# Kernel optimization log

Measured on AMD Instinct MI355X. Metric: run time of the kernel, lower is better.

The kernel has to match this reference:

```python
import jax, jax.numpy as jnp
import numpy as np

N0, N1, N2 = 262144, 65536, 16384   # sampled src nodes, layer-1 targets, layer-2 targets
E1, E2 = 1048576, 262144            # fanout 16 edges per layer
IN_C, HID_C, OUT_C = 128, 256, 64


def sage_conv(x_src, x_dst, src, dst, num_dst, W_l, W_r, b):
    # PyG SAGEConv (mean aggr): out = mean_{j in N(i)} x_src[j] @ W_l^T + b + x_dst @ W_r^T
    msgs = x_src[src]                                   # [E, C] gather
    s = jax.ops.segment_sum(msgs, dst, num_segments=num_dst)
    cnt = jax.ops.segment_sum(jnp.ones((src.shape[0],), x_src.dtype), dst,
                              num_segments=num_dst)
    aggr = s / jnp.maximum(cnt, 1.0)[:, None]           # mean; isolated nodes -> 0
    return aggr @ W_l.T + b + x_dst @ W_r.T


def setup_inputs() -> dict:
    key = jax.random.key(0)
    ks = jax.random.split(key, 9)
    inp = {
        "x": jax.random.normal(ks[0], (N0, IN_C), dtype=jnp.float32),
        "src1": jax.random.randint(ks[1], (E1,), 0, N0, dtype=jnp.int32),
        "dst1": jax.random.randint(ks[2], (E1,), 0, N1, dtype=jnp.int32),
        "src2": jax.random.randint(ks[3], (E2,), 0, N1, dtype=jnp.int32),
        "dst2": jax.random.randint(ks[4], (E2,), 0, N2, dtype=jnp.int32),
        "W1_l": jax.random.normal(ks[5], (HID_C, IN_C), dtype=jnp.float32) * 0.05,
        "W1_r": jax.random.normal(ks[6], (HID_C, IN_C), dtype=jnp.float32) * 0.05,
        "b1": jnp.zeros((HID_C,), dtype=jnp.float32),
        "W2_l": jax.random.normal(ks[7], (OUT_C, HID_C), dtype=jnp.float32) * 0.05,
        "W2_r": jax.random.normal(ks[8], (OUT_C, HID_C), dtype=jnp.float32) * 0.05,
        "b2": jnp.zeros((OUT_C,), dtype=jnp.float32),
    }
    return inp


def reference(x, src1, dst1, src2, dst2, W1_l, W1_r, b1, W2_l, W2_r, b2):
    # layer 1: sources = all N0 nodes, targets = first N1 nodes (x_target = x[:size[1]])
    h = sage_conv(x, x[:N1], src1, dst1, N1, W1_l, W1_r, b1)   # [N1, HID_C]
    h = jax.nn.relu(h)   # dropout is identity in eval mode
    # layer 2: sources = N1 layer-1 outputs, targets = first N2
    h = sage_conv(h, h[:N2], src2, dst2, N2, W2_l, W2_r, b2)   # [N2, OUT_C]
    return jax.nn.log_softmax(h, axis=-1)
```

## Files before the change

### kernel.cpp

```cpp
#include <hip/hip_runtime.h>
#include <cstdint>
#include <cstddef>

#define N0C 262144
#define N1C 65536
#define N2C 16384
#define E1C 1048576
#define E2C 262144

typedef __attribute__((ext_vector_type(8))) short bf16x8;
typedef __attribute__((ext_vector_type(4))) float f32x4;

__device__ __forceinline__ unsigned short f2bf(float f) {
  union { float f; unsigned u; } q; q.f = f;
  unsigned r = q.u + 0x7fffu + ((q.u >> 16) & 1u);
  return (unsigned short)(r >> 16);
}
__device__ __forceinline__ float blo(unsigned u) {
  union { unsigned u; float f; } q; q.u = u << 16; return q.f;
}
__device__ __forceinline__ float bhi(unsigned u) {
  union { unsigned u; float f; } q; q.u = u & 0xffff0000u; return q.f;
}
__device__ __forceinline__ void gl_lds16(const void* g, void* l) {
  __builtin_amdgcn_global_load_lds((const __attribute__((address_space(1))) void*)g,
                                   (__attribute__((address_space(3))) void*)l, 16, 0, 0);
}

__global__ void cvtx_kernel(const float4* __restrict__ in, ushort4* __restrict__ out, int n4) {
  int i = blockIdx.x * blockDim.x + threadIdx.x;
  int stride = gridDim.x * blockDim.x;
  for (; i < n4; i += stride) {
    float4 v = in[i];
    ushort4 o;
    o.x = f2bf(v.x); o.y = f2bf(v.y); o.z = f2bf(v.z); o.w = f2bf(v.w);
    out[i] = o;
  }
}

__global__ __launch_bounds__(256) void cvtw_kernel(
    const float4* __restrict__ W1l, const float4* __restrict__ W1r,
    const float4* __restrict__ W2l, const float4* __restrict__ W2r,
    ushort4* __restrict__ W1lb, ushort4* __restrict__ W1rb,
    ushort4* __restrict__ W2lb, ushort4* __restrict__ W2rb,
    int* __restrict__ btail) {
  int y = blockIdx.y;
  int i = blockIdx.x * 256 + threadIdx.x;
  if (y == 4) {
    if (i < 512) btail[i] = 0;
    return;
  }
  const float4* in; ushort4* outp; int n4;
  if (y == 0)      { in = W1l; outp = W1lb; n4 = 8192; }
  else if (y == 1) { in = W1r; outp = W1rb; n4 = 8192; }
  else if (y == 2) { in = W2l; outp = W2lb; n4 = 4096; }
  else             { in = W2r; outp = W2rb; n4 = 4096; }
  if (i < n4) {
    float4 v = in[i];
    ushort4 o;
    o.x = f2bf(v.x); o.y = f2bf(v.y); o.z = f2bf(v.z); o.w = f2bf(v.w);
    outp[i] = o;
  }
}

__global__ __launch_bounds__(256) void binA_kernel(
    const int* __restrict__ src1, const int* __restrict__ dst1,
    const int* __restrict__ src2, const int* __restrict__ dst2,
    int* __restrict__ btail, uint2* __restrict__ pair1, uint2* __restrict__ pair2) {
  __shared__ int hist[256];
  __shared__ int lofs[256];
  __shared__ int gbase[256];
  __shared__ int sstg[4096];
  __shared__ int dstg[4096];
  int b = blockIdx.x;
  int t = threadIdx.x;
  const int* src; const int* dst; int shift; int* bt; uint2* pb; int e0;
  if (b < 256) { src = src1; dst = dst1; shift = 8; bt = btail;       pb = pair1; e0 = b * 4096; }
  else         { src = src2; dst = dst2; shift = 6; bt = btail + 256; pb = pair2; e0 = (b - 256) * 4096; }
  hist[t] = 0;
  __syncthreads();
  int s_[16], d_[16], rk[16];
#pragma unroll
  for (int k = 0; k < 16; ++k) {
    int e = e0 + k * 256 + t;
    s_[k] = src[e];
    d_[k] = dst[e];
    rk[k] = atomicAdd(&hist[d_[k] >> shift], 1);
  }
  __syncthreads();
  int v = hist[t];
  lofs[t] = v;
  __syncthreads();
  for (int ofs = 1; ofs < 256; ofs <<= 1) {
    int add = (t >= ofs) ? lofs[t - ofs] : 0;
    __syncthreads();
    lofs[t] += add;
    __syncthreads();
  }
  gbase[t] = atomicAdd(&bt[t], v);
  int excl = lofs[t] - v;
  lofs[t] = excl;
  __syncthreads();
#pragma unroll
  for (int k = 0; k < 16; ++k) {
    int p = lofs[d_[k] >> shift] + rk[k];
    sstg[p] = s_[k];
    dstg[p] = d_[k];
  }
  __syncthreads();
  for (int i = t; i < 4096; i += 256) {
    int d = dstg[i];
    int bk = d >> shift;
    int idx = gbase[bk] + (i - lofs[bk]);
    if (idx < 8192)
      pb[(size_t)bk * 8192 + idx] = make_uint2((unsigned)sstg[i], (unsigned)d);
  }
}

__global__ __launch_bounds__(256) void binB_kernel(
    const uint2* __restrict__ pair1, const uint2* __restrict__ pair2,
    const int* __restrict__ btail,
    int* __restrict__ off1, int* __restrict__ cnt1, int* __restrict__ ssrc1,
    int* __restrict__ off2, int* __restrict__ cnt2, int* __restrict__ ssrc2) {
  __shared__ int lcnt[256];
  __shared__ int loff[256];
  __shared__ int lcnt2[256];
  __shared__ int stage[8192];
  int b = blockIdx.x;
  int t = threadIdx.x;
  const uint2* pb; const int* bt; int dpb; int* off; int* cnt; int* ssrc; int bl;
  if (b < 256) { bl = b;       pb = pair1 + (size_t)bl * 8192; bt = btail;       dpb = 256; off = off1; cnt = cnt1; ssrc = ssrc1; }
  else         { bl = b - 256; pb = pair2 + (size_t)bl * 8192; bt = btail + 256; dpb = 64;  off = off2; cnt = cnt2; ssrc = ssrc2; }
  lcnt[t] = (t < bl) ? bt[t] : 0;
  __syncthreads();
  for (int ofs = 128; ofs > 0; ofs >>= 1) {
    if (t < ofs) lcnt[t] += lcnt[t + ofs];
    __syncthreads();
  }
  int base = lcnt[0];
  __syncthreads();
  lcnt[t] = 0;
  lcnt2[t] = 0;
  __syncthreads();
  int n = bt[bl];
  if (n > 8192) n = 8192;
  for (int i = t; i < n; i += 256) {
    uint2 p = pb[i];
    atomicAdd(&lcnt[p.y & (dpb - 1)], 1);
  }
  __syncthreads();
  int v = lcnt[t];
  loff[t] = v;
  __syncthreads();
  for (int ofs = 1; ofs < 256; ofs <<= 1) {
    int add = (t >= ofs) ? loff[t - ofs] : 0;
    __syncthreads();
    loff[t] += add;
    __syncthreads();
  }
  int excl = loff[t] - v;
  loff[t] = excl;
  if (t < dpb) {
    cnt[bl * dpb + t] = v;
    off[bl * dpb + t] = base + excl;
  }
  __syncthreads();
  for (int i = t; i < n; i += 256) {
    uint2 p = pb[i];
    int dl = p.y & (dpb - 1);
    int r = atomicAdd(&lcnt2[dl], 1);
    stage[loff[dl] + r] = (int)p.x;
  }
  __syncthreads();
  for (int i = t; i < n; i += 256) ssrc[base + i] = stage[i];
}

__global__ __launch_bounds__(256) void agg1_kernel(const ushort* __restrict__ xb,
                                                   const int* __restrict__ ssrc,
                                                   const int* __restrict__ off,
                                                   const int* __restrict__ cnt,
                                                   ushort* __restrict__ aggr) {
  int wid = (blockIdx.x * 256 + threadIdx.x) >> 6;
  int lane = threadIdx.x & 63;
  int grp = lane >> 4;
  int cl = lane & 15;
  int start = __builtin_amdgcn_readfirstlane(off[wid]);
  int n = __builtin_amdgcn_readfirstlane(cnt[wid]);
  float a0 = 0.f, a1 = 0.f, a2 = 0.f, a3 = 0.f, a4 = 0.f, a5 = 0.f, a6 = 0.f, a7 = 0.f;
  int j = 0;
  for (; j + 4 <= n; j += 4) {
    int s = ssrc[start + j + grp];
    uint4 v = *(const uint4*)(xb + (size_t)s * 128 + cl * 8);
    a0 += blo(v.x); a1 += bhi(v.x); a2 += blo(v.y); a3 += bhi(v.y);
    a4 += blo(v.z); a5 += bhi(v.z); a6 += blo(v.w); a7 += bhi(v.w);
  }
  if (grp < n - j) {
    int s = ssrc[start + j + grp];
    uint4 v = *(const uint4*)(xb + (size_t)s * 128 + cl * 8);
    a0 += blo(v.x); a1 += bhi(v.x); a2 += blo(v.y); a3 += bhi(v.y);
    a4 += blo(v.z); a5 += bhi(v.z); a6 += blo(v.w); a7 += bhi(v.w);
  }
#define RED1(v) v += __shfl_xor(v, 16); v += __shfl_xor(v, 32);
  RED1(a0) RED1(a1) RED1(a2) RED1(a3) RED1(a4) RED1(a5) RED1(a6) RED1(a7)
#undef RED1
  if (lane < 16) {
    float inv = (n > 0) ? 1.0f / (float)n : 0.f;
    uint4 o;
    o.x = (unsigned)f2bf(a0 * inv) | ((unsigned)f2bf(a1 * inv) << 16);
    o.y = (unsigned)f2bf(a2 * inv) | ((unsigned)f2bf(a3 * inv) << 16);
    o.z = (unsigned)f2bf(a4 * inv) | ((unsigned)f2bf(a5 * inv) << 16);
    o.w = (unsigned)f2bf(a6 * inv) | ((unsigned)f2bf(a7 * inv) << 16);
    *(uint4*)(aggr + (size_t)wid * 128 + cl * 8) = o;
  }
}

__global__ __launch_bounds__(256) void agg2_kernel(const ushort* __restrict__ h1b,
                                                   const int* __restrict__ ssrc,
                                                   const int* __restrict__ off,
                                                   const int* __restrict__ cnt,
                                                   ushort* __restrict__ aggr) {
  int wid = (blockIdx.x * 256 + threadIdx.x) >> 6;
  int lane = threadIdx.x & 63;
  int grp = lane >> 5;
  int cl = lane & 31;
  int start = __builtin_amdgcn_readfirstlane(off[wid]);
  int n = __builtin_amdgcn_readfirstlane(cnt[wid]);
  float a0 = 0.f, a1 = 0.f, a2 = 0.f, a3 = 0.f, a4 = 0.f, a5 = 0.f, a6 = 0.f, a7 = 0.f;
  int j = 0;
  for (; j + 4 <= n; j += 4) {
    int sa = ssrc[start + j + grp];
    int sb = ssrc[start + j + 2 + grp];
    uint4 va = *(const uint4*)(h1b + (size_t)sa * 256 + cl * 8);
    uint4 vb = *(const uint4*)(h1b + (size_t)sb * 256 + cl * 8);
    a0 += blo(va.x) + blo(vb.x); a1 += bhi(va.x) + bhi(vb.x);
    a2 += blo(va.y) + blo(vb.y); a3 += bhi(va.y) + bhi(vb.y);
    a4 += blo(va.z) + blo(vb.z); a5 += bhi(va.z) + bhi(vb.z);
    a6 += blo(va.w) + blo(vb.w); a7 += bhi(va.w) + bhi(vb.w);
  }
  if (j + 2 <= n) {
    int s = ssrc[start + j + grp];
    uint4 v = *(const uint4*)(h1b + (size_t)s * 256 + cl * 8);
    a0 += blo(v.x); a1 += bhi(v.x); a2 += blo(v.y); a3 += bhi(v.y);
    a4 += blo(v.z); a5 += bhi(v.z); a6 += blo(v.w); a7 += bhi(v.w);
    j += 2;
  }
  if (grp < n - j) {
    int s = ssrc[start + j + grp];
    uint4 v = *(const uint4*)(h1b + (size_t)s * 256 + cl * 8);
    a0 += blo(v.x); a1 += bhi(v.x); a2 += blo(v.y); a3 += bhi(v.y);
    a4 += blo(v.z); a5 += bhi(v.z); a6 += blo(v.w); a7 += bhi(v.w);
  }
#define RED2(v) v += __shfl_xor(v, 32);
  RED2(a0) RED2(a1) RED2(a2) RED2(a3) RED2(a4) RED2(a5) RED2(a6) RED2(a7)
#undef RED2
  if (lane < 32) {
    float inv = (n > 0) ? 1.0f / (float)n : 0.f;
    uint4 o;
    o.x = (unsigned)f2bf(a0 * inv) | ((unsigned)f2bf(a1 * inv) << 16);
    o.y = (unsigned)f2bf(a2 * inv) | ((unsigned)f2bf(a3 * inv) << 16);
    o.z = (unsigned)f2bf(a4 * inv) | ((unsigned)f2bf(a5 * inv) << 16);
    o.w = (unsigned)f2bf(a6 * inv) | ((unsigned)f2bf(a7 * inv) << 16);
    *(uint4*)(aggr + (size_t)wid * 256 + cl * 8) = o;
  }
}

__global__ __launch_bounds__(512) void mgemm1_kernel(
    const ushort* __restrict__ aggr1, const ushort* __restrict__ xb,
    const ushort* __restrict__ W1lb, const ushort* __restrict__ W1rb,
    const float* __restrict__ b1, ushort* __restrict__ h1b) {
  __shared__ ushort smem[24576];
  ushort* sA = smem;
  ushort* sB = smem + 8192;
  int t = threadIdx.x;
  int lane = t & 63;
  int w = t >> 6;
  int wm = w >> 2, wn = w & 3;
  int i0 = blockIdx.x * 128;

  int sr = t >> 3;
  int sc = (t & 7) ^ (sr & 7);
  int quad = lane >> 4;
  int l15 = lane & 15;
  int xorv = lane & 7;

  f32x4 acc[4][4];
#pragma unroll
  for (int i = 0; i < 4; ++i)
#pragma unroll
    for (int j = 0; j < 4; ++j) acc[i][j] = (f32x4)(0.f);

  for (int kt = 0; kt < 4; ++kt) {
    const ushort* Asrc = (kt < 2) ? aggr1 : xb;
    const ushort* Bsrc = (kt < 2) ? W1lb : W1rb;
    int koff = (kt & 1) * 64;
#pragma unroll
    for (int it = 0; it < 2; ++it) {
      int r = it * 64 + sr;
      gl_lds16(Asrc + (size_t)(i0 + r) * 128 + koff + sc * 8, sA + (it * 512 + t) * 8);
    }
#pragma unroll
    for (int it = 0; it < 4; ++it) {
      int r = it * 64 + sr;
      gl_lds16(Bsrc + (size_t)r * 128 + koff + sc * 8, sB + (it * 512 + t) * 8);
    }
    __syncthreads();
#pragma unroll
    for (int s = 0; s < 2; ++s) {
      int chunk = ((s * 4 + quad) ^ xorv) * 8;
      bf16x8 av[4], bv[4];
#pragma unroll
      for (int fi = 0; fi < 4; ++fi)
        av[fi] = *(const bf16x8*)(sA + (wm * 64 + fi * 16 + l15) * 64 + chunk);
#pragma unroll
      for (int fj = 0; fj < 4; ++fj)
        bv[fj] = *(const bf16x8*)(sB + (wn * 64 + fj * 16 + l15) * 64 + chunk);
#pragma unroll
      for (int fi = 0; fi < 4; ++fi)
#pragma unroll
        for (int fj = 0; fj < 4; ++fj)
          acc[fi][fj] = __builtin_amdgcn_mfma_f32_16x16x32_bf16(av[fi], bv[fj], acc[fi][fj], 0, 0, 0);
    }
    __syncthreads();
  }

  for (int ph = 0; ph < 2; ++ph) {
    if (wm == ph) {
      ushort* eb = smem + (w & 3) * 4096;
#pragma unroll
      for (int fj = 0; fj < 4; ++fj) {
        float bias = b1[wn * 64 + fj * 16 + l15];
#pragma unroll
        for (int fi = 0; fi < 4; ++fi)
#pragma unroll
          for (int r = 0; r < 4; ++r) {
            float v = fmaxf(acc[fi][fj][r] + bias, 0.f);
            eb[(fi * 16 + quad * 4 + r) * 64 + fj * 16 + l15] = f2bf(v);
          }
      }
#pragma unroll
      for (int i = 0; i < 16; ++i) {
        int row = i * 4 + (lane >> 4);
        uint2 v = *(const uint2*)(eb + row * 64 + l15 * 4);
        *(uint2*)(h1b + (size_t)(i0 + wm * 64 + row) * 256 + wn * 64 + l15 * 4) = v;
      }
    }
    __syncthreads();
  }
}

__global__ __launch_bounds__(256) void mgemm2_kernel(
    const ushort* __restrict__ aggr2, const ushort* __restrict__ h1b,
    const ushort* __restrict__ W2lb, const ushort* __restrict__ W2rb,
    const float* __restrict__ b2, float* __restrict__ out) {
  __shared__ ushort sA[64 * 64];
  __shared__ ushort sB[64 * 64];
  int t = threadIdx.x;
  int lane = t & 63;
  int w = t >> 6;
  int i0 = blockIdx.x * 64;

  int sr = t >> 3;
  int sc = (t & 7) ^ (sr & 7);
  int quad = lane >> 4;
  int l15 = lane & 15;
  int xorv = lane & 7;

  f32x4 acc[4];
#pragma unroll
  for (int j = 0; j < 4; ++j) acc[j] = (f32x4)(0.f);

  for (int kt = 0; kt < 8; ++kt) {
    const ushort* Asrc = (kt < 4) ? aggr2 : h1b;
    const ushort* Bsrc = (kt < 4) ? W2lb : W2rb;
    int koff = (kt & 3) * 64;
#pragma unroll
    for (int it = 0; it < 2; ++it) {
      int r = it * 32 + sr;
      gl_lds16(Asrc + (size_t)(i0 + r) * 256 + koff + sc * 8, sA + (it * 256 + t) * 8);
    }
#pragma unroll
    for (int it = 0; it < 2; ++it) {
      int r = it * 32 + sr;
      gl_lds16(Bsrc + (size_t)r * 256 + koff + sc * 8, sB + (it * 256 + t) * 8);
    }
    __syncthreads();
#pragma unroll
    for (int s = 0; s < 2; ++s) {
      int chunk = ((s * 4 + quad) ^ xorv) * 8;
      bf16x8 av = *(const bf16x8*)(sA + (w * 16 + l15) * 64 + chunk);
      bf16x8 bv[4];
#pragma unroll
      for (int fj = 0; fj < 4; ++fj)
        bv[fj] = *(const bf16x8*)(sB + (fj * 16 + l15) * 64 + chunk);
#pragma unroll
      for (int fj = 0; fj < 4; ++fj)
        acc[fj] = __builtin_amdgcn_mfma_f32_16x16x32_bf16(av, bv[fj], acc[fj], 0, 0, 0);
    }
    __syncthreads();
  }

  float b2c[4];
#pragma unroll
  for (int fj = 0; fj < 4; ++fj) b2c[fj] = b2[fj * 16 + l15];

#pragma unroll
  for (int r = 0; r < 4; ++r) {
    int row = i0 + w * 16 + quad * 4 + r;
    float v[4];
#pragma unroll
    for (int fj = 0; fj < 4; ++fj) v[fj] = acc[fj][r] + b2c[fj];
    float m = fmaxf(fmaxf(v[0], v[1]), fmaxf(v[2], v[3]));
    m = fmaxf(m, __shfl_xor(m, 1));
    m = fmaxf(m, __shfl_xor(m, 2));
    m = fmaxf(m, __shfl_xor(m, 4));
    m = fmaxf(m, __shfl_xor(m, 8));
    float ssum = __expf(v[0] - m) + __expf(v[1] - m) + __expf(v[2] - m) + __expf(v[3] - m);
    ssum += __shfl_xor(ssum, 1);
    ssum += __shfl_xor(ssum, 2);
    ssum += __shfl_xor(ssum, 4);
    ssum += __shfl_xor(ssum, 8);
    float lg = m + __logf(ssum);
#pragma unroll
    for (int fj = 0; fj < 4; ++fj)
      out[(size_t)row * 64 + fj * 16 + l15] = v[fj] - lg;
  }
}


extern "C" void kernel_launch(void* const* d_in, const int* in_sizes, int n_in,
                              void* d_out, int out_size, void* d_ws, size_t ws_size,
                              hipStream_t stream) {
  const float* x   = (const float*)d_in[0];
  const int* src1  = (const int*)d_in[1];
  const int* dst1  = (const int*)d_in[2];
  const int* src2  = (const int*)d_in[3];
  const int* dst2  = (const int*)d_in[4];
  const float* W1l = (const float*)d_in[5];
  const float* W1r = (const float*)d_in[6];
  const float* b1  = (const float*)d_in[7];
  const float* W2l = (const float*)d_in[8];
  const float* W2r = (const float*)d_in[9];
  const float* b2  = (const float*)d_in[10];
  float* out = (float*)d_out;

  char* base = (char*)d_ws;
  ushort* xb   = (ushort*)base;
  ushort* ag1b = (ushort*)(base + 67108864);
  ushort* ag2b = (ushort*)(base + 83886080);
  uint2* pair1 = (uint2*)(base + 92274688);
  uint2* pair2 = (uint2*)(base + 109051904);
  ushort* h1b  = (ushort*)(base + 92274688);
  int* cnt1  = (int*)(base + 125829120);
  int* off1  = cnt1 + N1C;
  int* cnt2  = off1 + N1C;
  int* off2  = cnt2 + N2C;
  int* btail = off2 + N2C;
  int* ssrc1 = btail + 512;
  int* ssrc2 = ssrc1 + E1C;
  ushort* W1lb = (ushort*)(ssrc2 + E2C);
  ushort* W1rb = W1lb + 32768;
  ushort* W2lb = W1rb + 32768;
  ushort* W2rb = W2lb + 16384;

  cvtw_kernel<<<dim3(32, 5), 256, 0, stream>>>(
      (const float4*)W1l, (const float4*)W1r, (const float4*)W2l, (const float4*)W2r,
      (ushort4*)W1lb, (ushort4*)W1rb, (ushort4*)W2lb, (ushort4*)W2rb, btail);

  cvtx_kernel<<<4096, 256, 0, stream>>>((const float4*)x, (ushort4*)xb, N0C * 128 / 4);

  binA_kernel<<<320, 256, 0, stream>>>(src1, dst1, src2, dst2, btail, pair1, pair2);
  binB_kernel<<<512, 256, 0, stream>>>(pair1, pair2, btail,
                                       off1, cnt1, ssrc1, off2, cnt2, ssrc2);

  agg1_kernel<<<N1C / 4, 256, 0, stream>>>(xb, ssrc1, off1, cnt1, ag1b);
  mgemm1_kernel<<<N1C / 128, 512, 0, stream>>>(ag1b, xb, W1lb, W1rb, b1, h1b);

  agg2_kernel<<<N2C / 4, 256, 0, stream>>>(h1b, ssrc2, off2, cnt2, ag2b);
  mgemm2_kernel<<<N2C / 64, 256, 0, stream>>>(ag2b, h1b, W2lb, W2rb, b2, out);
}
```

Baseline: 167.1 us.

## Fuse x bf16 conversion into binning kernel, pack edge pairs, unroll gathers

Merges the x-to-bf16 conversion and the first binning pass into one launch. Extra blocks handle the conversion while the binning blocks run alongside them. Edge pairs are packed into a single 32-bit word holding the local destination in the high bits and the source in the low 18 bits, which halves pair traffic and LDS staging. The workspace layout is moved so that h1b no longer overlaps the pair buffers. The aggregation loops are also unrolled further to keep more gathers in flight, at the cost of more registers and tail handling.

```diff
diff --git a/kernel.cpp b/kernel.cpp
--- a/kernel.cpp
+++ b/kernel.cpp
@@ -25,17 +25,6 @@
 __device__ __forceinline__ void gl_lds16(const void* g, void* l) {
   __builtin_amdgcn_global_load_lds((const __attribute__((address_space(1))) void*)g,
                                    (__attribute__((address_space(3))) void*)l, 16, 0, 0);
-}
-
-__global__ void cvtx_kernel(const float4* __restrict__ in, ushort4* __restrict__ out, int n4) {
-  int i = blockIdx.x * blockDim.x + threadIdx.x;
-  int stride = gridDim.x * blockDim.x;
-  for (; i < n4; i += stride) {
-    float4 v = in[i];
-    ushort4 o;
-    o.x = f2bf(v.x); o.y = f2bf(v.y); o.z = f2bf(v.z); o.w = f2bf(v.w);
-    out[i] = o;
-  }
 }
 
 __global__ __launch_bounds__(256) void cvtw_kernel(
@@ -63,29 +52,44 @@
   }
 }
 
-__global__ __launch_bounds__(256) void binA_kernel(
+__global__ __launch_bounds__(256) void mega_kernel(
     const int* __restrict__ src1, const int* __restrict__ dst1,
     const int* __restrict__ src2, const int* __restrict__ dst2,
-    int* __restrict__ btail, uint2* __restrict__ pair1, uint2* __restrict__ pair2) {
+    int* __restrict__ btail, unsigned* __restrict__ pair1, unsigned* __restrict__ pair2,
+    const float4* __restrict__ x, ushort4* __restrict__ xb) {
   __shared__ int hist[256];
   __shared__ int lofs[256];
   __shared__ int gbase[256];
-  __shared__ int sstg[4096];
-  __shared__ int dstg[4096];
+  __shared__ unsigned stg[4096];
+  __shared__ unsigned char bstg[4096];
   int b = blockIdx.x;
   int t = threadIdx.x;
-  const int* src; const int* dst; int shift; int* bt; uint2* pb; int e0;
-  if (b < 256) { src = src1; dst = dst1; shift = 8; bt = btail;       pb = pair1; e0 = b * 4096; }
-  else         { src = src2; dst = dst2; shift = 6; bt = btail + 256; pb = pair2; e0 = (b - 256) * 4096; }
+  if (b >= 320) {
+    int i = (b - 320) * 256 + t;
+    const int stride = 2048 * 256;
+    const int n4 = N0C * 128 / 4;
+    for (; i < n4; i += stride) {
+      float4 v = x[i];
+      ushort4 o;
+      o.x = f2bf(v.x); o.y = f2bf(v.y); o.z = f2bf(v.z); o.w = f2bf(v.w);
+      xb[i] = o;
+    }
+    return;
+  }
+  const int* src; const int* dst; int shift; int dmask; int* bt; unsigned* pb; int e0;
+  if (b < 256) { src = src1; dst = dst1; shift = 8; dmask = 255; bt = btail;       pb = pair1; e0 = b * 4096; }
+  else         { src = src2; dst = dst2; shift = 6; dmask = 63;  bt = btail + 256; pb = pair2; e0 = (b - 256) * 4096; }
   hist[t] = 0;
   __syncthreads();
-  int s_[16], d_[16], rk[16];
+  unsigned pk[16]; int bk[16], rk[16];
 #pragma unroll
   for (int k = 0; k < 16; ++k) {
     int e = e0 + k * 256 + t;
-    s_[k] = src[e];
-    d_[k] = dst[e];
-    rk[k] = atomicAdd(&hist[d_[k] >> shift], 1);
+    int s = src[e];
+    int d = dst[e];
+    bk[k] = d >> shift;
+    pk[k] = ((unsigned)(d & dmask) << 18) | (unsigned)s;
+    rk[k] = atomicAdd(&hist[bk[k]], 1);
   }
   __syncthreads();
   int v = hist[t];
@@ -103,32 +107,31 @@
   __syncthreads();
 #pragma unroll
   for (int k = 0; k < 16; ++k) {
-    int p = lofs[d_[k] >> shift] + rk[k];
-    sstg[p] = s_[k];
-    dstg[p] = d_[k];
+    int p = lofs[bk[k]] + rk[k];
+    stg[p] = pk[k];
+    bstg[p] = (unsigned char)bk[k];
   }
   __syncthreads();
   for (int i = t; i < 4096; i += 256) {
-    int d = dstg[i];
-    int bk = d >> shift;
-    int idx = gbase[bk] + (i - lofs[bk]);
+    int bki = bstg[i];
+    int idx = gbase[bki] + (i - lofs[bki]);
     if (idx < 8192)
-      pb[(size_t)bk * 8192 + idx] = make_uint2((unsigned)sstg[i], (unsigned)d);
+      pb[(size_t)bki * 8192 + idx] = stg[i];
   }
 }
 
 __global__ __launch_bounds__(256) void binB_kernel(
-    const uint2* __restrict__ pair1, const uint2* __restrict__ pair2,
+    const unsigned* __restrict__ pair1, const unsigned* __restrict__ pair2,
     const int* __restrict__ btail,
     int* __restrict__ off1, int* __restrict__ cnt1, int* __restrict__ ssrc1,
     int* __restrict__ off2, int* __restrict__ cnt2, int* __restrict__ ssrc2) {
   __shared__ int lcnt[256];
   __shared__ int loff[256];
   __shared__ int lcnt2[256];
-  __shared__ int stage[8192];
+  __shared__ unsigned stage[8192];
   int b = blockIdx.x;
   int t = threadIdx.x;
-  const uint2* pb; const int* bt; int dpb; int* off; int* cnt; int* ssrc; int bl;
+  const unsigned* pb; const int* bt; int dpb; int* off; int* cnt; int* ssrc; int bl;
   if (b < 256) { bl = b;       pb = pair1 + (size_t)bl * 8192; bt = btail;       dpb = 256; off = off1; cnt = cnt1; ssrc = ssrc1; }
   else         { bl = b - 256; pb = pair2 + (size_t)bl * 8192; bt = btail + 256; dpb = 64;  off = off2; cnt = cnt2; ssrc = ssrc2; }
   lcnt[t] = (t < bl) ? bt[t] : 0;
@@ -145,8 +148,8 @@
   int n = bt[bl];
   if (n > 8192) n = 8192;
   for (int i = t; i < n; i += 256) {
-    uint2 p = pb[i];
-    atomicAdd(&lcnt[p.y & (dpb - 1)], 1);
+    unsigned p = pb[i];
+    atomicAdd(&lcnt[p >> 18], 1);
   }
   __syncthreads();
   int v = lcnt[t];
@@ -166,13 +169,13 @@
   }
   __syncthreads();
   for (int i = t; i < n; i += 256) {
-    uint2 p = pb[i];
-    int dl = p.y & (dpb - 1);
+    unsigned p = pb[i];
+    int dl = p >> 18;
     int r = atomicAdd(&lcnt2[dl], 1);
-    stage[loff[dl] + r] = (int)p.x;
-  }
-  __syncthreads();
-  for (int i = t; i < n; i += 256) ssrc[base + i] = stage[i];
+    stage[loff[dl] + r] = p & 0x3FFFFu;
+  }
+  __syncthreads();
+  for (int i = t; i < n; i += 256) ssrc[base + i] = (int)stage[i];
 }
 
 __global__ __launch_bounds__(256) void agg1_kernel(const ushort* __restrict__ xb,
@@ -188,11 +191,22 @@
   int n = __builtin_amdgcn_readfirstlane(cnt[wid]);
   float a0 = 0.f, a1 = 0.f, a2 = 0.f, a3 = 0.f, a4 = 0.f, a5 = 0.f, a6 = 0.f, a7 = 0.f;
   int j = 0;
-  for (; j + 4 <= n; j += 4) {
+  for (; j + 8 <= n; j += 8) {
+    int sa = ssrc[start + j + grp];
+    int sb = ssrc[start + j + 4 + grp];
+    uint4 va = *(const uint4*)(xb + (size_t)sa * 128 + cl * 8);
+    uint4 vb = *(const uint4*)(xb + (size_t)sb * 128 + cl * 8);
+    a0 += blo(va.x) + blo(vb.x); a1 += bhi(va.x) + bhi(vb.x);
+    a2 += blo(va.y) + blo(vb.y); a3 += bhi(va.y) + bhi(vb.y);
+    a4 += blo(va.z) + blo(vb.z); a5 += bhi(va.z) + bhi(vb.z);
+    a6 += blo(va.w) + blo(vb.w); a7 += bhi(va.w) + bhi(vb.w);
+  }
+  if (j + 4 <= n) {
     int s = ssrc[start + j + grp];
     uint4 v = *(const uint4*)(xb + (size_t)s * 128 + cl * 8);
     a0 += blo(v.x); a1 += bhi(v.x); a2 += blo(v.y); a3 += bhi(v.y);
     a4 += blo(v.z); a5 += bhi(v.z); a6 += blo(v.w); a7 += bhi(v.w);
+    j += 4;
   }
   if (grp < n - j) {
     int s = ssrc[start + j + grp];
@@ -227,22 +241,29 @@
   int n = __builtin_amdgcn_readfirstlane(cnt[wid]);
   float a0 = 0.f, a1 = 0.f, a2 = 0.f, a3 = 0.f, a4 = 0.f, a5 = 0.f, a6 = 0.f, a7 = 0.f;
   int j = 0;
-  for (; j + 4 <= n; j += 4) {
-    int sa = ssrc[start + j + grp];
-    int sb = ssrc[start + j + 2 + grp];
-    uint4 va = *(const uint4*)(h1b + (size_t)sa * 256 + cl * 8);
-    uint4 vb = *(const uint4*)(h1b + (size_t)sb * 256 + cl * 8);
-    a0 += blo(va.x) + blo(vb.x); a1 += bhi(va.x) + bhi(vb.x);
-    a2 += blo(va.y) + blo(vb.y); a3 += bhi(va.y) + bhi(vb.y);
-    a4 += blo(va.z) + blo(vb.z); a5 += bhi(va.z) + bhi(vb.z);
-    a6 += blo(va.w) + blo(vb.w); a7 += bhi(va.w) + bhi(vb.w);
-  }
-  if (j + 2 <= n) {
+  for (; j + 8 <= n; j += 8) {
+    int s0 = ssrc[start + j + grp];
+    int s1 = ssrc[start + j + 2 + grp];
+    int s2 = ssrc[start + j + 4 + grp];
+    int s3 = ssrc[start + j + 6 + grp];
+    uint4 v0 = *(const uint4*)(h1b + (size_t)s0 * 256 + cl * 8);
+    uint4 v1 = *(const uint4*)(h1b + (size_t)s1 * 256 + cl * 8);
+    uint4 v2 = *(const uint4*)(h1b + (size_t)s2 * 256 + cl * 8);
+    uint4 v3 = *(const uint4*)(h1b + (size_t)s3 * 256 + cl * 8);
+    a0 += blo(v0.x) + blo(v1.x) + blo(v2.x) + blo(v3.x);
+    a1 += bhi(v0.x) + bhi(v1.x) + bhi(v2.x) + bhi(v3.x);
+    a2 += blo(v0.y) + blo(v1.y) + blo(v2.y) + blo(v3.y);
+    a3 += bhi(v0.y) + bhi(v1.y) + bhi(v2.y) + bhi(v3.y);
+    a4 += blo(v0.z) + blo(v1.z) + blo(v2.z) + blo(v3.z);
+    a5 += bhi(v0.z) + bhi(v1.z) + bhi(v2.z) + bhi(v3.z);
+    a6 += blo(v0.w) + blo(v1.w) + blo(v2.w) + blo(v3.w);
+    a7 += bhi(v0.w) + bhi(v1.w) + bhi(v2.w) + bhi(v3.w);
+  }
+  for (; j + 2 <= n; j += 2) {
     int s = ssrc[start + j + grp];
     uint4 v = *(const uint4*)(h1b + (size_t)s * 256 + cl * 8);
     a0 += blo(v.x); a1 += bhi(v.x); a2 += blo(v.y); a3 += bhi(v.y);
     a4 += blo(v.z); a5 += bhi(v.z); a6 += blo(v.w); a7 += bhi(v.w);
-    j += 2;
   }
   if (grp < n - j) {
     int s = ssrc[start + j + grp];
@@ -447,10 +468,10 @@
   ushort* xb   = (ushort*)base;
   ushort* ag1b = (ushort*)(base + 67108864);
   ushort* ag2b = (ushort*)(base + 83886080);
-  uint2* pair1 = (uint2*)(base + 92274688);
-  uint2* pair2 = (uint2*)(base + 109051904);
-  ushort* h1b  = (ushort*)(base + 92274688);
-  int* cnt1  = (int*)(base + 125829120);
+  unsigned* pair1 = (unsigned*)(base + 92274688);
+  unsigned* pair2 = (unsigned*)(base + 100663296);
+  ushort* h1b  = (ushort*)(base + 109051904);
+  int* cnt1  = (int*)(base + 142606336);
   int* off1  = cnt1 + N1C;
   int* cnt2  = off1 + N1C;
   int* off2  = cnt2 + N2C;
@@ -466,9 +487,9 @@
       (const float4*)W1l, (const float4*)W1r, (const float4*)W2l, (const float4*)W2r,
       (ushort4*)W1lb, (ushort4*)W1rb, (ushort4*)W2lb, (ushort4*)W2rb, btail);
 
-  cvtx_kernel<<<4096, 256, 0, stream>>>((const float4*)x, (ushort4*)xb, N0C * 128 / 4);
-
-  binA_kernel<<<320, 256, 0, stream>>>(src1, dst1, src2, dst2, btail, pair1, pair2);
+  mega_kernel<<<2368, 256, 0, stream>>>(src1, dst1, src2, dst2, btail, pair1, pair2,
+                                        (const float4*)x, (ushort4*)xb);
+
   binB_kernel<<<512, 256, 0, stream>>>(pair1, pair2, btail,
                                        off1, cnt1, ssrc1, off2, cnt2, ssrc2);
 
```

New measurement: 154.1 us. 7.8% less time.
